# Kernel optimization log

Hardware: AMD Instinct MI355X
Metric: run time of the kernel (lower is better)

The kernel has to match this reference:

```python
import jax, jax.numpy as jnp
import numpy as np

DIM = 1024
HEADS = 16
GROUPS = 4
DIM_HEAD = 64
INNER = HEADS * DIM_HEAD  # 1024
KV_DIM = 2 * DIM_HEAD * GROUPS  # 512
B, N = 4, 2048
EPS = 1e-6


def _layernorm(x, scale, bias, eps=EPS):
    mu = jnp.mean(x, axis=-1, keepdims=True)
    var = jnp.mean(jnp.square(x - mu), axis=-1, keepdims=True)
    return (x - mu) * jax.lax.rsqrt(var + eps) * scale + bias


def setup_inputs() -> dict:
    key = jax.random.key(0)
    ks = jax.random.split(key, 10)
    lecun = lambda k, shape: jax.random.normal(k, shape, jnp.float32) * (1.0 / np.sqrt(shape[0]))
    return {
        "x": jax.random.normal(ks[0], (B, N, DIM), jnp.float32),
        "ln_scale": jnp.ones((DIM,), jnp.float32),
        "ln_bias": jnp.zeros((DIM,), jnp.float32),
        "Wq": lecun(ks[1], (DIM, INNER)),
        "Wkv": lecun(ks[2], (DIM, KV_DIM)),
        "qn_scale": jnp.ones((DIM_HEAD,), jnp.float32),
        "qn_bias": jnp.zeros((DIM_HEAD,), jnp.float32),
        "kn_scale": jnp.ones((DIM_HEAD,), jnp.float32),
        "kn_bias": jnp.zeros((DIM_HEAD,), jnp.float32),
        "Wout": lecun(ks[3], (INNER, DIM)),
    }


def reference(x, ln_scale, ln_bias, Wq, Wkv, qn_scale, qn_bias, kn_scale, kn_bias, Wout):
    b, n, _ = x.shape
    g, hg, d = GROUPS, HEADS // GROUPS, DIM_HEAD
    scale = d ** -0.5
    xn = _layernorm(x, ln_scale, ln_bias)
    # q: (b,n,inner) -> (b,h,n,d)
    q = (xn @ Wq).reshape(b, n, HEADS, d).transpose(0, 2, 1, 3)
    kv = xn @ Wkv
    k, v = jnp.split(kv, 2, axis=-1)
    # (b,n,g*d) -> (b,g,n,d)
    k = k.reshape(b, n, g, d).transpose(0, 2, 1, 3)
    v = v.reshape(b, n, g, d).transpose(0, 2, 1, 3)
    q = _layernorm(q, qn_scale, qn_bias)
    k = _layernorm(k, kn_scale, kn_bias)
    # split heads into groups: (b, g*hg, n, d) -> (b, g, hg, n, d)
    qg = q.reshape(b, g, hg, n, d)
    dots = jnp.einsum('bghqd,bgkd->bghqk', qg, k) * scale
    attn = jax.nn.softmax(dots, axis=-1)
    out = jnp.einsum('bghqk,bgkd->bghqd', attn, v)  # (b,g,hg,n,d)
    out = out.transpose(0, 3, 1, 2, 4).reshape(b, n, g * hg * d)
    return out @ Wout
```

## Files before the change

### kernel.cpp

```cpp
#include <hip/hip_runtime.h>
#include <cstdint>
#include <cstddef>

typedef unsigned short u16;
typedef __attribute__((ext_vector_type(4))) float f32x4;
typedef __attribute__((ext_vector_type(8))) __bf16 bf16x8;
typedef __attribute__((ext_vector_type(4))) __bf16 bf16x4;
typedef __attribute__((ext_vector_type(8))) unsigned short u16x8;

#define DEV static __device__ __forceinline__

#if __has_builtin(__builtin_amdgcn_exp2f)
#define EXP2(x) __builtin_amdgcn_exp2f(x)
#else
#define EXP2(x) exp2f(x)
#endif

DEV float bf2f(u16 v) { return __uint_as_float(((unsigned)v) << 16); }
DEV u16 f2bf(float f) {
  unsigned u = __float_as_uint(f);
  return (u16)((u + 0x7FFFu + ((u >> 16) & 1u)) >> 16);
}

DEV void gl_lds16(const void* g, void* l) {
  __builtin_amdgcn_global_load_lds((const __attribute__((address_space(1))) void*)g,
                                   (__attribute__((address_space(3))) void*)l, 16, 0, 0);
}

__global__ __launch_bounds__(256) void trans_qkv_w(const float* __restrict__ Wq,
                                                   const float* __restrict__ Wkv,
                                                   u16* __restrict__ bt) {
  __shared__ __attribute__((aligned(16))) u16 t[64 * 72];
  const int r0 = blockIdx.x * 64, tid = threadIdx.x;
  const int by = blockIdx.y;
  const float* in;
  int incols, c0;
  u16* out;
  if (by < 16) { in = Wq; incols = 1024; c0 = by * 64; out = bt; }
  else { in = Wkv; incols = 512; c0 = (by - 16) * 64; out = bt + 1024 * 1024; }
#pragma unroll
  for (int i = 0; i < 2; i++) {
    int c = i * 256 + tid;
    int row = c >> 3, cc = c & 7;
    const float* src = &in[(size_t)(r0 + row) * incols + c0 + cc * 8];
    f32x4 v0 = *(const f32x4*)src;
    f32x4 v1 = *(const f32x4*)(src + 4);
    u16x8 o;
#pragma unroll
    for (int j = 0; j < 4; j++) { o[j] = f2bf(v0[j]); o[4 + j] = f2bf(v1[j]); }
    *(u16x8*)&t[row * 72 + cc * 8] = o;
  }
  __syncthreads();
#pragma unroll
  for (int i = 0; i < 2; i++) {
    int c = i * 256 + tid;
    int d = c >> 3, nc = c & 7;
    u16x8 o;
#pragma unroll
    for (int j = 0; j < 8; j++) o[j] = t[(nc * 8 + j) * 72 + d];
    *(u16x8*)&out[(size_t)(c0 + d) * 1024 + r0 + nc * 8] = o;
  }
}

__global__ __launch_bounds__(256) void transpose64(const float* __restrict__ in,
                                                   u16* __restrict__ out, int incols) {
  __shared__ __attribute__((aligned(16))) u16 t[64 * 72];
  const int r0 = blockIdx.x * 64, c0 = blockIdx.y * 64, tid = threadIdx.x;
#pragma unroll
  for (int i = 0; i < 2; i++) {
    int c = i * 256 + tid;
    int row = c >> 3, cc = c & 7;
    const float* src = &in[(size_t)(r0 + row) * incols + c0 + cc * 8];
    f32x4 v0 = *(const f32x4*)src;
    f32x4 v1 = *(const f32x4*)(src + 4);
    u16x8 o;
#pragma unroll
    for (int j = 0; j < 4; j++) { o[j] = f2bf(v0[j]); o[4 + j] = f2bf(v1[j]); }
    *(u16x8*)&t[row * 72 + cc * 8] = o;
  }
  __syncthreads();
#pragma unroll
  for (int i = 0; i < 2; i++) {
    int c = i * 256 + tid;
    int d = c >> 3, nc = c & 7;
    u16x8 o;
#pragma unroll
    for (int j = 0; j < 8; j++) o[j] = t[(nc * 8 + j) * 72 + d];
    *(u16x8*)&out[(size_t)(c0 + d) * 1024 + r0 + nc * 8] = o;
  }
}

__global__ __launch_bounds__(256) void ln_x(const float* __restrict__ x,
                                            const float* __restrict__ sc,
                                            const float* __restrict__ bi,
                                            u16* __restrict__ xn) {
  __shared__ float red[8];
  const int row = blockIdx.x, tid = threadIdx.x;
  const int w = tid >> 6;
  f32x4 f = *(const f32x4*)&x[(size_t)row * 1024 + tid * 4];
  float s = f[0] + f[1] + f[2] + f[3];
  float q = f[0] * f[0] + f[1] * f[1] + f[2] * f[2] + f[3] * f[3];
#pragma unroll
  for (int off = 1; off < 64; off <<= 1) {
    s += __shfl_xor(s, off);
    q += __shfl_xor(q, off);
  }
  if ((tid & 63) == 0) { red[w] = s; red[4 + w] = q; }
  __syncthreads();
  float S = red[0] + red[1] + red[2] + red[3];
  float Q = red[4] + red[5] + red[6] + red[7];
  float mu = S * (1.0f / 1024.0f);
  float var = Q * (1.0f / 1024.0f) - mu * mu;
  float rs = rsqrtf(var + 1e-6f);
  f32x4 scv = *(const f32x4*)&sc[tid * 4];
  f32x4 biv = *(const f32x4*)&bi[tid * 4];
  u16* o = xn + (size_t)row * 1024 + tid * 4;
#pragma unroll
  for (int j = 0; j < 4; j++) o[j] = f2bf((f[j] - mu) * rs * scv[j] + biv[j]);
}

template <bool F32OUT>
__global__ __launch_bounds__(256) void gemm_bt(const u16* __restrict__ A,
                                               const u16* __restrict__ Bt,
                                               void* __restrict__ Cp,
                                               int M, int N, int K) {
  __shared__ __attribute__((aligned(16))) u16 Als[128 * 64];
  __shared__ __attribute__((aligned(16))) u16 Bls[128 * 64];
  const int tid = threadIdx.x;
  const int w = tid >> 6, lane = tid & 63, ln = lane & 15, quad = lane >> 4;
  const int m0 = blockIdx.y * 128, n0 = blockIdx.x * 128;
  const int moff = (w & 1) * 64, noff = (w >> 1) * 64;
  const f32x4 fzero = {0.f, 0.f, 0.f, 0.f};
  f32x4 acc[4][4];
#pragma unroll
  for (int i = 0; i < 4; i++)
#pragma unroll
    for (int j = 0; j < 4; j++) acc[i][j] = fzero;

  const u16* aS[4];
  const u16* bS[4];
#pragma unroll
  for (int i = 0; i < 4; i++) {
    int s = i * 256 + tid;
    int row = s >> 3, cs = (s & 7) ^ (row & 7);
    aS[i] = A + (size_t)(m0 + row) * K + cs * 8;
    bS[i] = Bt + (size_t)(n0 + row) * K + cs * 8;
  }

  for (int k0 = 0; k0 < K; k0 += 64) {
    __syncthreads();
#pragma unroll
    for (int i = 0; i < 4; i++) {
      int s = i * 256 + tid;
      gl_lds16(aS[i] + k0, &Als[s * 8]);
      gl_lds16(bS[i] + k0, &Bls[s * 8]);
    }
    __syncthreads();
#pragma unroll
    for (int kk = 0; kk < 2; kk++) {
      bf16x8 af[4], bfv[4];
#pragma unroll
      for (int mi = 0; mi < 4; mi++)
        af[mi] = *(const bf16x8*)
            &Als[(moff + mi * 16 + ln) * 64 + (((kk * 4 + quad) ^ (ln & 7)) * 8)];
#pragma unroll
      for (int ni = 0; ni < 4; ni++)
        bfv[ni] = *(const bf16x8*)
            &Bls[(noff + ni * 16 + ln) * 64 + (((kk * 4 + quad) ^ (ln & 7)) * 8)];
#pragma unroll
      for (int mi = 0; mi < 4; mi++)
#pragma unroll
        for (int ni = 0; ni < 4; ni++)
          acc[mi][ni] = __builtin_amdgcn_mfma_f32_16x16x32_bf16(af[mi], bfv[ni],
                                                                acc[mi][ni], 0, 0, 0);
    }
  }
#pragma unroll
  for (int mi = 0; mi < 4; mi++)
#pragma unroll
    for (int ni = 0; ni < 4; ni++)
#pragma unroll
      for (int r = 0; r < 4; r++) {
        size_t m = m0 + moff + mi * 16 + quad * 4 + r;
        size_t n = n0 + noff + ni * 16 + ln;
        if (F32OUT)
          ((float*)Cp)[m * N + n] = acc[mi][ni][r];
        else
          ((u16*)Cp)[m * N + n] = f2bf(acc[mi][ni][r]);
      }
}

__global__ __launch_bounds__(256) void qkv_post(const u16* __restrict__ qkv,
                                                const float* __restrict__ qs,
                                                const float* __restrict__ qb,
                                                const float* __restrict__ ks,
                                                const float* __restrict__ kb,
                                                u16* __restrict__ Q,
                                                u16* __restrict__ Kb,
                                                u16* __restrict__ Vt) {
  __shared__ __attribute__((aligned(16))) u16 t[64 * 72];
  const int bid = blockIdx.x;
  const int tid = threadIdx.x;
  if (bid < 8192) {
    const float SCL = 0.18033688011112042f;
    const int b = bid >> 11, n = bid & 2047;
    const int w = tid >> 6, lane = tid & 63;
    const u16* rowp = qkv + (size_t)bid * 1536;
    const float qsc = qs[lane], qbi = qb[lane];
    const float ksc = ks[lane], kbi = kb[lane];
#pragma unroll
    for (int i = 0; i < 4; i++) {
      int h = w * 4 + i;
      float v = bf2f(rowp[h * 64 + lane]);
      float s = v, q2 = v * v;
#pragma unroll
      for (int off = 1; off < 64; off <<= 1) {
        s += __shfl_xor(s, off);
        q2 += __shfl_xor(q2, off);
      }
      float mu = s * (1.0f / 64.0f);
      float var = q2 * (1.0f / 64.0f) - mu * mu;
      float y = ((v - mu) * rsqrtf(var + 1e-6f) * qsc + qbi) * SCL;
      Q[((size_t)(b * 16 + h) * 2048 + n) * 64 + lane] = f2bf(y);
    }
    {
      int g = w;
      float v = bf2f(rowp[1024 + g * 64 + lane]);
      float s = v, q2 = v * v;
#pragma unroll
      for (int off = 1; off < 64; off <<= 1) {
        s += __shfl_xor(s, off);
        q2 += __shfl_xor(q2, off);
      }
      float mu = s * (1.0f / 64.0f);
      float var = q2 * (1.0f / 64.0f) - mu * mu;
      float y = (v - mu) * rsqrtf(var + 1e-6f) * ksc + kbi;
      Kb[((size_t)(b * 4 + g) * 2048 + n) * 64 + lane] = f2bf(y);
    }
  } else {
    const int idx = bid - 8192;
    const int n0 = (idx & 31) * 64;
    const int bg = idx >> 5;
    const int b = bg >> 2, g = bg & 3;
    const u16* src = qkv + (size_t)(b * 2048 + n0) * 1536 + 1280 + g * 64;
#pragma unroll
    for (int i = 0; i < 2; i++) {
      int c = i * 256 + tid;
      int row = c >> 3, cc = c & 7;
      *(f32x4*)&t[row * 72 + cc * 8] = *(const f32x4*)&src[(size_t)row * 1536 + cc * 8];
    }
    __syncthreads();
    u16* dst = Vt + (size_t)bg * 64 * 2048 + n0;
#pragma unroll
    for (int i = 0; i < 2; i++) {
      int c = i * 256 + tid;
      int d = c >> 3, nc = c & 7;
      u16x8 o;
#pragma unroll
      for (int j = 0; j < 8; j++) o[j] = t[(nc * 8 + j) * 72 + d];
      *(u16x8*)&dst[(size_t)d * 2048 + nc * 8] = o;
    }
  }
}

__global__ __launch_bounds__(256, 5) void attn(const u16* __restrict__ Q,
                                               const u16* __restrict__ Kb,
                                               const u16* __restrict__ Vt,
                                               u16* __restrict__ Out) {
  __shared__ __attribute__((aligned(16))) u16 Kls[64 * 64];
  __shared__ __attribute__((aligned(16))) u16 Vls[64 * 64];
  __shared__ __attribute__((aligned(16))) u16 Pls[4][16 * 64];
  const int qt = blockIdx.x;
  const int bh = blockIdx.y;
  const int b = bh >> 4, h = bh & 15, g = h >> 2;
  const int tid = threadIdx.x, w = tid >> 6, lane = tid & 63;
  const int ln = lane & 15, quad = lane >> 4;
  const u16* Qg = Q + ((size_t)(b * 16 + h) * 2048 + qt * 64 + w * 16) * 64;
  const u16* Kg = Kb + (size_t)(b * 4 + g) * 2048 * 64;
  const u16* Vg = Vt + (size_t)(b * 4 + g) * 64 * 2048;
  const f32x4 fzero = {0.f, 0.f, 0.f, 0.f};

  bf16x8 qf[2];
#pragma unroll
  for (int ks2 = 0; ks2 < 2; ks2++)
    qf[ks2] = *(const bf16x8*)&Qg[(size_t)ln * 64 + ks2 * 32 + quad * 8];

  f32x4 oacc[4];
#pragma unroll
  for (int ni = 0; ni < 4; ni++) oacc[ni] = fzero;
  float lsum = 0.f;
  u16* Pw = &Pls[w][0];

  const int sk0 = tid, sk1 = 256 + tid;
  const int krow0 = sk0 >> 3, kcs0 = (sk0 & 7) ^ (krow0 & 7);
  const int krow1 = sk1 >> 3, kcs1 = (sk1 & 7) ^ (krow1 & 7);
  const u16* kp0 = Kg + (size_t)krow0 * 64 + kcs0 * 8;
  const u16* kp1 = Kg + (size_t)krow1 * 64 + kcs1 * 8;
  const u16* vp0 = Vg + (size_t)krow0 * 2048 + kcs0 * 8;
  const u16* vp1 = Vg + (size_t)krow1 * 2048 + kcs1 * 8;
  u16* kd0 = &Kls[sk0 * 8];
  u16* kd1 = &Kls[sk1 * 8];
  u16* vd0 = &Vls[sk0 * 8];
  u16* vd1 = &Vls[sk1 * 8];
  int koffA[4], koffB[4], vroff[4][2];
#pragma unroll
  for (int ni = 0; ni < 4; ni++) {
    const int row = ni * 16 + ln;
    koffA[ni] = row * 64 + ((quad ^ (ln & 7)) * 8);
    koffB[ni] = row * 64 + (((4 + quad) ^ (ln & 7)) * 8);
#pragma unroll
    for (int kc = 0; kc < 2; kc++)
      vroff[ni][kc] = row * 64 + (((4 * kc + quad) ^ (ln & 7)) * 8);
  }
  char* pst[4];
#pragma unroll
  for (int ni = 0; ni < 4; ni++)
    pst[ni] = (char*)Pw + ln * 128 + (((2 * ni + (quad >> 1)) ^ (ln & 7)) * 16) +
              ((quad & 1) * 8);
  int proff[2];
#pragma unroll
  for (int kc = 0; kc < 2; kc++)
    proff[kc] = ln * 64 + (((4 * kc + quad) ^ (ln & 7)) * 8);

  for (int kt = 0; kt < 32; kt++) {
    __syncthreads();
    gl_lds16(kp0, kd0);
    gl_lds16(kp1, kd1);
    gl_lds16(vp0, vd0);
    gl_lds16(vp1, vd1);
    kp0 += 64 * 64; kp1 += 64 * 64;
    vp0 += 64; vp1 += 64;
    __syncthreads();

    f32x4 sacc[4];
#pragma unroll
    for (int ni = 0; ni < 4; ni++) {
      bf16x8 kf0 = *(const bf16x8*)&Kls[koffA[ni]];
      bf16x8 kf1 = *(const bf16x8*)&Kls[koffB[ni]];
      f32x4 tt = __builtin_amdgcn_mfma_f32_16x16x32_bf16(kf0, qf[0], fzero, 0, 0, 0);
      sacc[ni] = __builtin_amdgcn_mfma_f32_16x16x32_bf16(kf1, qf[1], tt, 0, 0, 0);
    }

    float ls = 0.f;
#pragma unroll
    for (int ni = 0; ni < 4; ni++) {
      float p0 = EXP2(sacc[ni][0]);
      float p1 = EXP2(sacc[ni][1]);
      float p2 = EXP2(sacc[ni][2]);
      float p3 = EXP2(sacc[ni][3]);
      ls += (p0 + p1) + (p2 + p3);
      bf16x4 pv = {(__bf16)p0, (__bf16)p1, (__bf16)p2, (__bf16)p3};
      *(bf16x4*)pst[ni] = pv;
    }
    ls += __shfl_xor(ls, 16);
    ls += __shfl_xor(ls, 32);
    lsum += ls;

#pragma unroll
    for (int kc = 0; kc < 2; kc++) {
      bf16x8 pf = *(const bf16x8*)&Pw[proff[kc]];
#pragma unroll
      for (int ni = 0; ni < 4; ni++) {
        bf16x8 vf = *(const bf16x8*)&Vls[vroff[ni][kc]];
        oacc[ni] = __builtin_amdgcn_mfma_f32_16x16x32_bf16(vf, pf, oacc[ni], 0, 0, 0);
      }
    }
  }

  const float inv = 1.0f / lsum;
  u16* Og = Out + ((size_t)b * 2048 + qt * 64 + w * 16 + ln) * 1024 + h * 64;
#pragma unroll
  for (int ni = 0; ni < 4; ni++) {
    bf16x4 ov = {(__bf16)(oacc[ni][0] * inv), (__bf16)(oacc[ni][1] * inv),
                 (__bf16)(oacc[ni][2] * inv), (__bf16)(oacc[ni][3] * inv)};
    *(bf16x4*)&Og[ni * 16 + quad * 4] = ov;
  }
}

extern "C" void kernel_launch(void* const* d_in, const int* in_sizes, int n_in,
                              void* d_out, int out_size, void* d_ws, size_t ws_size,
                              hipStream_t stream) {
  const float* x    = (const float*)d_in[0];
  const float* lns  = (const float*)d_in[1];
  const float* lnb  = (const float*)d_in[2];
  const float* Wq   = (const float*)d_in[3];
  const float* Wkv  = (const float*)d_in[4];
  const float* qns  = (const float*)d_in[5];
  const float* qnb  = (const float*)d_in[6];
  const float* kns  = (const float*)d_in[7];
  const float* knb  = (const float*)d_in[8];
  const float* Wout = (const float*)d_in[9];
  float* out = (float*)d_out;
  char* ws = (char*)d_ws;

  const size_t o_xn  = 0;
  const size_t o_qkv = 16777216;
  const size_t o_bt  = o_qkv + 25165824;
  const size_t o_k   = o_bt + 3145728;
  const size_t o_vt  = o_k + 4194304;
  u16* xn   = (u16*)(ws + o_xn);
  u16* qkv  = (u16*)(ws + o_qkv);
  u16* bt   = (u16*)(ws + o_bt);
  u16* Kbuf = (u16*)(ws + o_k);
  u16* Vtb  = (u16*)(ws + o_vt);
  u16* Qbuf = xn;
  u16* aout = qkv;

  trans_qkv_w<<<dim3(16, 24), 256, 0, stream>>>(Wq, Wkv, bt);
  ln_x<<<8192, 256, 0, stream>>>(x, lns, lnb, xn);
  gemm_bt<false><<<dim3(12, 64), 256, 0, stream>>>(xn, bt, qkv, 8192, 1536, 1024);
  transpose64<<<dim3(16, 16), 256, 0, stream>>>(Wout, bt, 1024);
  qkv_post<<<8704, 256, 0, stream>>>(qkv, qns, qnb, kns, knb, Qbuf, Kbuf, Vtb);
  attn<<<dim3(32, 64), 256, 0, stream>>>(Qbuf, Kbuf, Vtb, aout);
  gemm_bt<true><<<dim3(8, 64), 256, 0, stream>>>(aout, bt, out, 8192, 1024, 1024);

  (void)in_sizes; (void)n_in; (void)out_size; (void)ws_size;
}
```

Measured before the change: 296.9 us.

## Split attention keys across waves with 128-key tiles and LDS reduction

The attention kernel now loads 128-key K/V tiles per iteration. Instead of each wave owning 16 query rows, every wave processes all 64 query rows against its own 32-key slice. K and V fragments read from LDS are reused across four query sub-tiles, so there are fewer LDS reads and loop iterations per MFMA. The price is more accumulator registers, lower target occupancy (launch bounds 3 instead of 5), and an epilogue that reduces the partial outputs and row sums of the four waves through LDS with extra barriers.

```diff
diff --git a/kernel.cpp b/kernel.cpp
--- a/kernel.cpp
+++ b/kernel.cpp
@@ -263,117 +263,180 @@
   }
 }
 
-__global__ __launch_bounds__(256, 5) void attn(const u16* __restrict__ Q,
+__global__ __launch_bounds__(256, 3) void attn(const u16* __restrict__ Q,
                                                const u16* __restrict__ Kb,
                                                const u16* __restrict__ Vt,
                                                u16* __restrict__ Out) {
-  __shared__ __attribute__((aligned(16))) u16 Kls[64 * 64];
-  __shared__ __attribute__((aligned(16))) u16 Vls[64 * 64];
-  __shared__ __attribute__((aligned(16))) u16 Pls[4][16 * 64];
+  __shared__ __attribute__((aligned(16))) u16 Kls[128 * 64];
+  __shared__ __attribute__((aligned(16))) u16 Vls[64 * 128];
+  __shared__ __attribute__((aligned(16))) u16 Pls[4][64 * 32];
   const int qt = blockIdx.x;
   const int bh = blockIdx.y;
   const int b = bh >> 4, h = bh & 15, g = h >> 2;
   const int tid = threadIdx.x, w = tid >> 6, lane = tid & 63;
   const int ln = lane & 15, quad = lane >> 4;
-  const u16* Qg = Q + ((size_t)(b * 16 + h) * 2048 + qt * 64 + w * 16) * 64;
+  const u16* Qg = Q + ((size_t)(b * 16 + h) * 2048 + qt * 64) * 64;
   const u16* Kg = Kb + (size_t)(b * 4 + g) * 2048 * 64;
   const u16* Vg = Vt + (size_t)(b * 4 + g) * 64 * 2048;
   const f32x4 fzero = {0.f, 0.f, 0.f, 0.f};
 
-  bf16x8 qf[2];
-#pragma unroll
-  for (int ks2 = 0; ks2 < 2; ks2++)
-    qf[ks2] = *(const bf16x8*)&Qg[(size_t)ln * 64 + ks2 * 32 + quad * 8];
-
-  f32x4 oacc[4];
-#pragma unroll
-  for (int ni = 0; ni < 4; ni++) oacc[ni] = fzero;
-  float lsum = 0.f;
+  bf16x8 qf[4][2];
+#pragma unroll
+  for (int mi = 0; mi < 4; mi++)
+#pragma unroll
+    for (int half = 0; half < 2; half++)
+      qf[mi][half] =
+          *(const bf16x8*)&Qg[(size_t)(mi * 16 + ln) * 64 + half * 32 + quad * 8];
+
+  f32x4 oacc[4][4];
+#pragma unroll
+  for (int ni = 0; ni < 4; ni++)
+#pragma unroll
+    for (int mi = 0; mi < 4; mi++) oacc[ni][mi] = fzero;
+  float lsum[4] = {0.f, 0.f, 0.f, 0.f};
   u16* Pw = &Pls[w][0];
 
-  const int sk0 = tid, sk1 = 256 + tid;
-  const int krow0 = sk0 >> 3, kcs0 = (sk0 & 7) ^ (krow0 & 7);
-  const int krow1 = sk1 >> 3, kcs1 = (sk1 & 7) ^ (krow1 & 7);
-  const u16* kp0 = Kg + (size_t)krow0 * 64 + kcs0 * 8;
-  const u16* kp1 = Kg + (size_t)krow1 * 64 + kcs1 * 8;
-  const u16* vp0 = Vg + (size_t)krow0 * 2048 + kcs0 * 8;
-  const u16* vp1 = Vg + (size_t)krow1 * 2048 + kcs1 * 8;
-  u16* kd0 = &Kls[sk0 * 8];
-  u16* kd1 = &Kls[sk1 * 8];
-  u16* vd0 = &Vls[sk0 * 8];
-  u16* vd1 = &Vls[sk1 * 8];
-  int koffA[4], koffB[4], vroff[4][2];
-#pragma unroll
-  for (int ni = 0; ni < 4; ni++) {
-    const int row = ni * 16 + ln;
-    koffA[ni] = row * 64 + ((quad ^ (ln & 7)) * 8);
-    koffB[ni] = row * 64 + (((4 + quad) ^ (ln & 7)) * 8);
-#pragma unroll
-    for (int kc = 0; kc < 2; kc++)
-      vroff[ni][kc] = row * 64 + (((4 * kc + quad) ^ (ln & 7)) * 8);
-  }
-  char* pst[4];
-#pragma unroll
-  for (int ni = 0; ni < 4; ni++)
-    pst[ni] = (char*)Pw + ln * 128 + (((2 * ni + (quad >> 1)) ^ (ln & 7)) * 16) +
-              ((quad & 1) * 8);
-  int proff[2];
-#pragma unroll
-  for (int kc = 0; kc < 2; kc++)
-    proff[kc] = ln * 64 + (((4 * kc + quad) ^ (ln & 7)) * 8);
-
-  for (int kt = 0; kt < 32; kt++) {
+  const u16* kp[4];
+  const u16* vp[4];
+#pragma unroll
+  for (int i = 0; i < 4; i++) {
+    int s = i * 256 + tid;
+    int key = s >> 3, ck = (s & 7) ^ (key & 7);
+    kp[i] = Kg + (size_t)key * 64 + ck * 8;
+    int d = s >> 4, cv = (s & 15) ^ (d & 15);
+    vp[i] = Vg + (size_t)d * 2048 + cv * 8;
+  }
+
+  const int swz2 = (ln >> 1) & 3;
+  const int kbase0 = (w * 32 + ln) * 64 + ((quad ^ (ln & 7)) * 8);
+  const int kbase1 = (w * 32 + ln) * 64 + (((4 + quad) ^ (ln & 7)) * 8);
+  const int vbase = ln * 128 + (((w * 4 + quad) ^ ln) * 8);
+  const int prbase = ln * 32 + ((quad ^ swz2) * 8);
+  char* pw0 = (char*)Pw + ln * 64 + (quad & 1) * 8 +
+              (((0 + (quad >> 1)) ^ swz2) * 16);
+  char* pw1 = (char*)Pw + ln * 64 + (quad & 1) * 8 +
+              (((2 + (quad >> 1)) ^ swz2) * 16);
+
+  for (int kt = 0; kt < 16; kt++) {
     __syncthreads();
-    gl_lds16(kp0, kd0);
-    gl_lds16(kp1, kd1);
-    gl_lds16(vp0, vd0);
-    gl_lds16(vp1, vd1);
-    kp0 += 64 * 64; kp1 += 64 * 64;
-    vp0 += 64; vp1 += 64;
+#pragma unroll
+    for (int i = 0; i < 4; i++) {
+      int s = i * 256 + tid;
+      gl_lds16(kp[i], &Kls[s * 8]);
+      kp[i] += 128 * 64;
+      gl_lds16(vp[i], &Vls[s * 8]);
+      vp[i] += 128;
+    }
     __syncthreads();
 
-    f32x4 sacc[4];
-#pragma unroll
-    for (int ni = 0; ni < 4; ni++) {
-      bf16x8 kf0 = *(const bf16x8*)&Kls[koffA[ni]];
-      bf16x8 kf1 = *(const bf16x8*)&Kls[koffB[ni]];
-      f32x4 tt = __builtin_amdgcn_mfma_f32_16x16x32_bf16(kf0, qf[0], fzero, 0, 0, 0);
-      sacc[ni] = __builtin_amdgcn_mfma_f32_16x16x32_bf16(kf1, qf[1], tt, 0, 0, 0);
-    }
-
-    float ls = 0.f;
-#pragma unroll
-    for (int ni = 0; ni < 4; ni++) {
-      float p0 = EXP2(sacc[ni][0]);
-      float p1 = EXP2(sacc[ni][1]);
-      float p2 = EXP2(sacc[ni][2]);
-      float p3 = EXP2(sacc[ni][3]);
-      ls += (p0 + p1) + (p2 + p3);
-      bf16x4 pv = {(__bf16)p0, (__bf16)p1, (__bf16)p2, (__bf16)p3};
-      *(bf16x4*)pst[ni] = pv;
-    }
-    ls += __shfl_xor(ls, 16);
-    ls += __shfl_xor(ls, 32);
-    lsum += ls;
-
-#pragma unroll
-    for (int kc = 0; kc < 2; kc++) {
-      bf16x8 pf = *(const bf16x8*)&Pw[proff[kc]];
-#pragma unroll
-      for (int ni = 0; ni < 4; ni++) {
-        bf16x8 vf = *(const bf16x8*)&Vls[vroff[ni][kc]];
-        oacc[ni] = __builtin_amdgcn_mfma_f32_16x16x32_bf16(vf, pf, oacc[ni], 0, 0, 0);
-      }
-    }
-  }
-
-  const float inv = 1.0f / lsum;
-  u16* Og = Out + ((size_t)b * 2048 + qt * 64 + w * 16 + ln) * 1024 + h * 64;
-#pragma unroll
-  for (int ni = 0; ni < 4; ni++) {
-    bf16x4 ov = {(__bf16)(oacc[ni][0] * inv), (__bf16)(oacc[ni][1] * inv),
-                 (__bf16)(oacc[ni][2] * inv), (__bf16)(oacc[ni][3] * inv)};
-    *(bf16x4*)&Og[ni * 16 + quad * 4] = ov;
+    f32x4 sacc[4][2];
+#pragma unroll
+    for (int ni2 = 0; ni2 < 2; ni2++) {
+      bf16x8 kf0 = *(const bf16x8*)&Kls[kbase0 + ni2 * 1024];
+      bf16x8 kf1 = *(const bf16x8*)&Kls[kbase1 + ni2 * 1024];
+#pragma unroll
+      for (int mi = 0; mi < 4; mi++) {
+        f32x4 tt = __builtin_amdgcn_mfma_f32_16x16x32_bf16(kf0, qf[mi][0], fzero, 0, 0, 0);
+        sacc[mi][ni2] = __builtin_amdgcn_mfma_f32_16x16x32_bf16(kf1, qf[mi][1], tt, 0, 0, 0);
+      }
+    }
+
+#pragma unroll
+    for (int mi = 0; mi < 4; mi++) {
+#pragma unroll
+      for (int ni2 = 0; ni2 < 2; ni2++) {
+        float p0 = EXP2(sacc[mi][ni2][0]);
+        float p1 = EXP2(sacc[mi][ni2][1]);
+        float p2 = EXP2(sacc[mi][ni2][2]);
+        float p3 = EXP2(sacc[mi][ni2][3]);
+        lsum[mi] += (p0 + p1) + (p2 + p3);
+        bf16x4 pv = {(__bf16)p0, (__bf16)p1, (__bf16)p2, (__bf16)p3};
+        *(bf16x4*)((ni2 ? pw1 : pw0) + mi * 1024) = pv;
+      }
+    }
+
+    bf16x8 vf[4];
+#pragma unroll
+    for (int ni = 0; ni < 4; ni++) vf[ni] = *(const bf16x8*)&Vls[vbase + ni * 2048];
+#pragma unroll
+    for (int mi = 0; mi < 4; mi++) {
+      bf16x8 pf = *(const bf16x8*)&Pw[prbase + mi * 512];
+#pragma unroll
+      for (int ni = 0; ni < 4; ni++)
+        oacc[ni][mi] = __builtin_amdgcn_mfma_f32_16x16x32_bf16(vf[ni], pf, oacc[ni][mi], 0, 0, 0);
+    }
+  }
+
+#pragma unroll
+  for (int mi = 0; mi < 4; mi++) {
+    float l = lsum[mi];
+    l += __shfl_xor(l, 16);
+    l += __shfl_xor(l, 32);
+    lsum[mi] = l;
+  }
+  __syncthreads();
+  float* regA = (float*)&Kls[0];
+  float* regB = (float*)&Vls[0];
+  float* lsArr = (float*)&Pls[0][0];
+  if (quad == 0) {
+#pragma unroll
+    for (int mi = 0; mi < 4; mi++) lsArr[w * 64 + mi * 16 + ln] = lsum[mi];
+  }
+  if (w >= 2) {
+    float* R = (w == 2) ? regA : regB;
+#pragma unroll
+    for (int ni = 0; ni < 4; ni++)
+#pragma unroll
+      for (int mi = 0; mi < 4; mi++)
+        *(f32x4*)&R[(ni * 4 + mi) * 256 + lane * 4] = oacc[ni][mi];
+  }
+  __syncthreads();
+  if (w == 0) {
+#pragma unroll
+    for (int ni = 0; ni < 4; ni++)
+#pragma unroll
+      for (int mi = 0; mi < 4; mi++)
+        oacc[ni][mi] += *(const f32x4*)&regA[(ni * 4 + mi) * 256 + lane * 4];
+#pragma unroll
+    for (int ni = 0; ni < 4; ni++)
+#pragma unroll
+      for (int mi = 0; mi < 4; mi++)
+        *(f32x4*)&regA[(ni * 4 + mi) * 256 + lane * 4] = oacc[ni][mi];
+  } else if (w == 1) {
+#pragma unroll
+    for (int ni = 0; ni < 4; ni++)
+#pragma unroll
+      for (int mi = 0; mi < 4; mi++)
+        oacc[ni][mi] += *(const f32x4*)&regB[(ni * 4 + mi) * 256 + lane * 4];
+#pragma unroll
+    for (int ni = 0; ni < 4; ni++)
+#pragma unroll
+      for (int mi = 0; mi < 4; mi++)
+        *(f32x4*)&regB[(ni * 4 + mi) * 256 + lane * 4] = oacc[ni][mi];
+  }
+  __syncthreads();
+  if (w < 2) {
+    float linv[4];
+#pragma unroll
+    for (int mi = 0; mi < 4; mi++) {
+      int m = mi * 16 + ln;
+      linv[mi] = 1.0f / (lsArr[m] + lsArr[64 + m] + lsArr[128 + m] + lsArr[192 + m]);
+    }
+    const float* other = (w == 0) ? regB : regA;
+    const int nlo = (w == 0) ? 0 : 2;
+#pragma unroll
+    for (int nn = 0; nn < 2; nn++) {
+      int ni = nlo + nn;
+#pragma unroll
+      for (int mi = 0; mi < 4; mi++) {
+        f32x4 o = oacc[ni][mi];
+        const f32x4 t2 = *(const f32x4*)&other[(ni * 4 + mi) * 256 + lane * 4];
+        bf16x4 ov = {(__bf16)((o[0] + t2[0]) * linv[mi]), (__bf16)((o[1] + t2[1]) * linv[mi]),
+                     (__bf16)((o[2] + t2[2]) * linv[mi]), (__bf16)((o[3] + t2[3]) * linv[mi])};
+        u16* Og = Out + ((size_t)b * 2048 + qt * 64 + mi * 16 + ln) * 1024 + h * 64;
+        *(bf16x4*)&Og[ni * 16 + quad * 4] = ov;
+      }
+    }
   }
 }
 
```

Measured after the change: 525.9 us. +77.1%, slower.
